# Optimization experiments

Hardware: AMD Instinct MI355X
Metric: run time of the kernel (lower is better)

Reference implementation:

```python
import jax, jax.numpy as jnp
import numpy as np

N = 50000          # num nodes
E = 800000         # num edges (avg degree 16)
H = 8              # num_heads
CH = [64, 64, 64, 32]  # [in_features] + conv_channels
EPS = 1e-5


def setup_inputs() -> dict:
    key = jax.random.key(0)
    ks = jax.random.split(key, 20)
    x = jax.random.normal(ks[0], (N, CH[0]), jnp.float32)
    src = jax.random.randint(ks[1], (E,), 0, N, dtype=jnp.int32)
    dst = jax.random.randint(ks[2], (E,), 0, N, dtype=jnp.int32)
    dst = jnp.where(src == dst, (dst + 1) % N, dst)  # no self-loops (remove_self_loops)
    edge_index = jnp.stack([src, dst])  # [2, E]

    def lin(k, shape):
        return jax.random.uniform(k, shape, jnp.float32) * 0.1

    inp = {"x": x, "edge_index": edge_index}
    ki = 3
    for layer, (cin, cout) in enumerate(zip(CH[:-1], CH[1:]), start=1):
        inp[f"W{layer}"] = lin(ks[ki], (H * cout, cin)); ki += 1
        inp[f"U{layer}"] = lin(ks[ki], (H, cin)); ki += 1
        inp[f"c{layer}"] = jax.random.normal(ks[ki], (H,), jnp.float32) * 0.1; ki += 1
        inp[f"b{layer}"] = jax.random.normal(ks[ki], (cout,), jnp.float32) * 0.1; ki += 1
        if layer < 3:  # batch norm on intermediate layers only
            inp[f"g{layer}"] = jnp.ones((cout,), jnp.float32)
            inp[f"be{layer}"] = jnp.zeros((cout,), jnp.float32)
    return inp


def _conv(x, src, dst, inv_count, W, U, c, b, out_ch):
    # FeatureSteeredConvolution (translation-invariant attention), mean aggr.
    xi = x[dst]                                   # [E2, Cin] target features
    xj = x[src]                                   # [E2, Cin] source features
    attn = jax.nn.softmax((xi - xj) @ U.T + c, axis=1)   # [E2, H]
    proj = (xj @ W.T).reshape(-1, H, out_ch)      # [E2, H, Cout]
    msg = jnp.einsum('eh,eho->eo', attn, proj)    # [E2, Cout]
    agg = jax.ops.segment_sum(msg, dst, num_segments=N) * inv_count[:, None]
    return agg + b


def _bn(x, g, be):
    # BatchNorm1d, training mode (batch stats, biased variance)
    m = x.mean(axis=0)
    v = ((x - m) ** 2).mean(axis=0)
    return g * (x - m) * jax.lax.rsqrt(v + EPS) + be


def reference(x, edge_index, W1, U1, c1, b1, g1, be1,
              W2, U2, c2, b2, g2, be2, W3, U3, c3, b3):
    loops = jnp.arange(N, dtype=edge_index.dtype)
    src = jnp.concatenate([edge_index[0], loops])  # add_self_loops
    dst = jnp.concatenate([edge_index[1], loops])
    count = jax.ops.segment_sum(jnp.ones_like(dst, jnp.float32), dst, num_segments=N)
    inv_count = 1.0 / count  # every node has its self-loop, so count >= 1

    h = _conv(x, src, dst, inv_count, W1, U1, c1, b1, CH[1])
    h = _bn(jax.nn.relu(h), g1, be1)
    h = _conv(h, src, dst, inv_count, W2, U2, c2, b2, CH[2])
    h = _bn(jax.nn.relu(h), g2, be2)
    return _conv(h, src, dst, inv_count, W3, U3, c3, b3, CH[3])
```

## Files before the change

### kernel.cpp

```cpp
#include <hip/hip_runtime.h>
#include <hip/hip_bf16.h>
#include <hip/hip_fp16.h>
#include <math.h>

constexpr int NN = 50000;
constexpr int NE = 800000;
constexpr float L2E = 1.44269504f;
constexpr int SBLK = 256;
constexpr int SGRID = (NN + SBLK - 1) / SBLK;

typedef __attribute__((ext_vector_type(8))) short bf16x8;
typedef __attribute__((ext_vector_type(4))) float f32x4;

__device__ inline float b2f(unsigned short u) {
  union { unsigned int i; float f; } v;
  v.i = ((unsigned int)u) << 16;
  return v.f;
}

__global__ void k_deg(const int* __restrict__ dst, int* __restrict__ degin) {
  int i = blockIdx.x * blockDim.x + threadIdx.x;
  if (i < NE) atomicAdd(&degin[dst[i]], 1);
}

__global__ void k_inv(const int* __restrict__ degin, float* __restrict__ inv) {
  int i = blockIdx.x * blockDim.x + threadIdx.x;
  if (i < NN) inv[i] = 1.0f / (float)(degin[i] + 1);
}

__global__ void k_scan1(const int* __restrict__ deg, int* __restrict__ bsum) {
  int i = blockIdx.x * SBLK + threadIdx.x;
  int v = (i < NN) ? deg[i] : 0;
#pragma unroll
  for (int off = 32; off; off >>= 1) v += __shfl_down(v, off, 64);
  __shared__ int ws[SBLK / 64];
  if ((threadIdx.x & 63) == 0) ws[threadIdx.x >> 6] = v;
  __syncthreads();
  if (threadIdx.x == 0) {
    int s = 0;
#pragma unroll
    for (int w = 0; w < SBLK / 64; ++w) s += ws[w];
    bsum[blockIdx.x] = s;
  }
}

__global__ void k_scan2(int* __restrict__ bsum) {
  __shared__ int ls[256];
  int t = threadIdx.x;
  int v = (t < SGRID) ? bsum[t] : 0;
  ls[t] = v;
  __syncthreads();
  for (int off = 1; off < 256; off <<= 1) {
    int u = (t >= off) ? ls[t - off] : 0;
    __syncthreads();
    ls[t] += u;
    __syncthreads();
  }
  if (t < SGRID) bsum[t] = ls[t] - v;
}

__global__ void k_scan3(const int* __restrict__ deg, const int* __restrict__ bsum,
                        int* __restrict__ base, int* __restrict__ cursor) {
  __shared__ int ls[SBLK];
  int t = threadIdx.x;
  int i = blockIdx.x * SBLK + t;
  int v = (i < NN) ? deg[i] : 0;
  ls[t] = v;
  __syncthreads();
  for (int off = 1; off < SBLK; off <<= 1) {
    int u = (t >= off) ? ls[t - off] : 0;
    __syncthreads();
    ls[t] += u;
    __syncthreads();
  }
  int ex = ls[t] - v + bsum[blockIdx.x];
  if (i < NN) { base[i] = ex; cursor[i] = ex; }
}

__global__ void k_scatter(const int* __restrict__ src, const int* __restrict__ dst,
                          int* __restrict__ cursor, int2* __restrict__ csc2) {
  int e = blockIdx.x * blockDim.x + threadIdx.x;
  if (e < NE) {
    int s = src[e], d = dst[e];
    int pos = atomicAdd(&cursor[d], 1);
    csc2[pos] = make_int2(s, d);
  }
}

__global__ void k_f2b(const float* __restrict__ in, __hip_bfloat16* __restrict__ out,
                      long n4) {
  long i = (long)blockIdx.x * blockDim.x + threadIdx.x;
  if (i >= n4) return;
  float4 v = reinterpret_cast<const float4*>(in)[i];
  ushort4 o;
  o.x = __hip_bfloat16_raw(__float2bfloat16(v.x)).x;
  o.y = __hip_bfloat16_raw(__float2bfloat16(v.y)).x;
  o.z = __hip_bfloat16_raw(__float2bfloat16(v.z)).x;
  o.w = __hip_bfloat16_raw(__float2bfloat16(v.w)).x;
  reinterpret_cast<ushort4*>(out)[i] = o;
}

__global__ void k_wt(const float* __restrict__ w1, const float* __restrict__ w2,
                     const float* __restrict__ w3, __hip_bfloat16* __restrict__ t1,
                     __hip_bfloat16* __restrict__ t2, __hip_bfloat16* __restrict__ t3) {
  int i = blockIdx.x * blockDim.x + threadIdx.x;
  const int n1 = 64 * 512, n2 = 64 * 512, n3 = 32 * 512;
  const float* w; __hip_bfloat16* t; int cout; int j = i;
  if (j < n1) { w = w1; t = t1; cout = 64; }
  else if ((j -= n1) < n2) { w = w2; t = t2; cout = 64; }
  else if ((j -= n2) < n3) { w = w3; t = t3; cout = 32; }
  else return;
  int o = j >> 9;
  int hc = j & 511;
  int h = hc >> 6, c = hc & 63;
  t[j] = __float2bfloat16(w[(h * cout + o) * 64 + c]);
}

__global__ void k_q(const float* __restrict__ X, const float* __restrict__ U,
                    float* __restrict__ q) {
  int n = blockIdx.x * blockDim.x + threadIdx.x;
  if (n >= NN) return;
  float4 xr[16];
  const float4* X4 = reinterpret_cast<const float4*>(X) + (size_t)n * 16;
#pragma unroll
  for (int i = 0; i < 16; ++i) xr[i] = X4[i];
  const float4* U4 = reinterpret_cast<const float4*>(U);
#pragma unroll
  for (int h = 0; h < 8; ++h) {
    float a = 0.f;
#pragma unroll
    for (int i = 0; i < 16; ++i) {
      float4 u = U4[h * 16 + i];
      a = fmaf(xr[i].x, u.x, a);
      a = fmaf(xr[i].y, u.y, a);
      a = fmaf(xr[i].z, u.z, a);
      a = fmaf(xr[i].w, u.w, a);
    }
    q[(size_t)n * 8 + h] = a * L2E;
  }
}

__global__ void k_attn(const int2* __restrict__ csc2, const float* __restrict__ q,
                       const float* __restrict__ cvec, const float* __restrict__ inv,
                       uint4* __restrict__ a) {
  int k = blockIdx.x * blockDim.x + threadIdx.x;
  if (k >= NE) return;
  int2 sd = csc2[k];
  int s = sd.x, d = sd.y;

  const float4* q4 = reinterpret_cast<const float4*>(q);
  const float4* c4 = reinterpret_cast<const float4*>(cvec);
  float4 qd0 = q4[2 * d], qd1 = q4[2 * d + 1];
  float4 qs0 = q4[2 * s], qs1 = q4[2 * s + 1];
  float4 c0 = c4[0], c1 = c4[1];

  float e[8];
  e[0] = __builtin_amdgcn_exp2f(qd0.x - qs0.x + c0.x * L2E);
  e[1] = __builtin_amdgcn_exp2f(qd0.y - qs0.y + c0.y * L2E);
  e[2] = __builtin_amdgcn_exp2f(qd0.z - qs0.z + c0.z * L2E);
  e[3] = __builtin_amdgcn_exp2f(qd0.w - qs0.w + c0.w * L2E);
  e[4] = __builtin_amdgcn_exp2f(qd1.x - qs1.x + c1.x * L2E);
  e[5] = __builtin_amdgcn_exp2f(qd1.y - qs1.y + c1.y * L2E);
  e[6] = __builtin_amdgcn_exp2f(qd1.z - qs1.z + c1.z * L2E);
  e[7] = __builtin_amdgcn_exp2f(qd1.w - qs1.w + c1.w * L2E);

  float sum = ((e[0] + e[1]) + (e[2] + e[3])) + ((e[4] + e[5]) + (e[6] + e[7]));
  float r = __builtin_amdgcn_rcpf(sum) * inv[d];

  __half2 h0 = __floats2half2_rn(e[0] * r, e[1] * r);
  __half2 h1 = __floats2half2_rn(e[2] * r, e[3] * r);
  __half2 h2 = __floats2half2_rn(e[4] * r, e[5] * r);
  __half2 h3 = __floats2half2_rn(e[6] * r, e[7] * r);
  uint4 o;
  o.x = *(unsigned int*)&h0;
  o.y = *(unsigned int*)&h1;
  o.z = *(unsigned int*)&h2;
  o.w = *(unsigned int*)&h3;
  a[k] = o;
}

#define ZACC(AV, XS)                                                      \
  do {                                                                    \
    float2 f0 = __half22float2(*(__half2*)&(AV).x);                       \
    float2 f1 = __half22float2(*(__half2*)&(AV).y);                       \
    float2 f2 = __half22float2(*(__half2*)&(AV).z);                       \
    float2 f3 = __half22float2(*(__half2*)&(AV).w);                       \
    z[0] = fmaf(f0.x, (XS), z[0]);                                        \
    z[1] = fmaf(f0.y, (XS), z[1]);                                        \
    z[2] = fmaf(f1.x, (XS), z[2]);                                        \
    z[3] = fmaf(f1.y, (XS), z[3]);                                        \
    z[4] = fmaf(f2.x, (XS), z[4]);                                        \
    z[5] = fmaf(f2.y, (XS), z[5]);                                        \
    z[6] = fmaf(f3.x, (XS), z[6]);                                        \
    z[7] = fmaf(f3.y, (XS), z[7]);                                        \
  } while (0)

__global__ void k_zagg(const int* __restrict__ cscbase, const int* __restrict__ cscend,
                       const int2* __restrict__ csc2, const uint4* __restrict__ a,
                       const ushort* __restrict__ xb, const float* __restrict__ inv,
                       const float* __restrict__ cvec, __hip_bfloat16* __restrict__ zb) {
  const int lane = threadIdx.x & 63;
  const int n = (int)(((long)blockIdx.x * blockDim.x + threadIdx.x) >> 6);
  if (n >= NN) return;

  float wc[8], wsum = 0.f;
#pragma unroll
  for (int h = 0; h < 8; ++h) { wc[h] = __builtin_amdgcn_exp2f(cvec[h] * L2E); wsum += wc[h]; }
  const float rxd = __builtin_amdgcn_rcpf(wsum) * inv[n] * b2f(xb[(size_t)n * 64 + lane]);
  float z[8];
#pragma unroll
  for (int h = 0; h < 8; ++h) z[h] = wc[h] * rxd;

  int k = cscbase[n];
  const int k1 = cscend[n];
  for (; k + 4 <= k1; k += 4) {
    int s0 = csc2[k + 0].x;
    int s1 = csc2[k + 1].x;
    int s2 = csc2[k + 2].x;
    int s3 = csc2[k + 3].x;
    uint4 a0 = a[k + 0];
    uint4 a1 = a[k + 1];
    uint4 a2 = a[k + 2];
    uint4 a3 = a[k + 3];
    float x0 = b2f(xb[(size_t)s0 * 64 + lane]);
    float x1 = b2f(xb[(size_t)s1 * 64 + lane]);
    float x2 = b2f(xb[(size_t)s2 * 64 + lane]);
    float x3 = b2f(xb[(size_t)s3 * 64 + lane]);
    ZACC(a0, x0);
    ZACC(a1, x1);
    ZACC(a2, x2);
    ZACC(a3, x3);
  }
  for (; k < k1; ++k) {
    int s = csc2[k].x;
    uint4 av = a[k];
    float xs = b2f(xb[(size_t)s * 64 + lane]);
    ZACC(av, xs);
  }

  ushort* zo = reinterpret_cast<ushort*>(zb) + (size_t)n * 512 + lane;
#pragma unroll
  for (int h = 0; h < 8; ++h)
    zo[h * 64] = __hip_bfloat16_raw(__float2bfloat16(z[h])).x;
}

template <int JOUT>
__global__ void __launch_bounds__(256)
k_zgemm(const __hip_bfloat16* __restrict__ Zb, const __hip_bfloat16* __restrict__ Wt,
        float* __restrict__ go) {
  const int lane = threadIdx.x & 63;
  const int w = threadIdx.x >> 6;
  const int m0 = (blockIdx.x * 4 + w) * 64;
  const int lr = lane & 15;
  const int lk = lane >> 4;
  constexpr int NT = JOUT / 16;

  const ushort* Z = reinterpret_cast<const ushort*>(Zb);
  const ushort* W = reinterpret_cast<const ushort*>(Wt);

  f32x4 acc[4][NT] = {};
  for (int kk = 0; kk < 16; ++kk) {
    bf16x8 bfr[NT];
#pragma unroll
    for (int ni = 0; ni < NT; ++ni) {
      int j = ni * 16 + lr;
      bfr[ni] = *reinterpret_cast<const bf16x8*>(W + (size_t)j * 512 + kk * 32 + lk * 8);
    }
#pragma unroll
    for (int mi = 0; mi < 4; ++mi) {
      int r = m0 + mi * 16 + lr;
      if (r >= NN) r = NN - 1;
      bf16x8 afr = *reinterpret_cast<const bf16x8*>(Z + (size_t)r * 512 + kk * 32 + lk * 8);
#pragma unroll
      for (int ni = 0; ni < NT; ++ni)
        acc[mi][ni] = __builtin_amdgcn_mfma_f32_16x16x32_bf16(afr, bfr[ni], acc[mi][ni], 0, 0, 0);
    }
  }

#pragma unroll
  for (int mi = 0; mi < 4; ++mi) {
#pragma unroll
    for (int i = 0; i < 4; ++i) {
      int r = m0 + mi * 16 + lk * 4 + i;
      if (r < NN) {
#pragma unroll
        for (int ni = 0; ni < NT; ++ni)
          go[(size_t)r * JOUT + ni * 16 + lr] = acc[mi][ni][i];
      }
    }
  }
}

__global__ void k_finalize_relu(const float* __restrict__ go, const float* __restrict__ b,
                                float* __restrict__ y, float* __restrict__ stats) {
  __shared__ float ssum[64], ssq[64];
  const int t = threadIdx.x;
  if (t < 64) { ssum[t] = 0.f; ssq[t] = 0.f; }
  __syncthreads();

  const int o = t & 63;
  const float bo = b[o];
  float lsum = 0.f, lsq = 0.f;
  for (long idx = (long)blockIdx.x * blockDim.x + threadIdx.x; idx < (long)NN * 64;
       idx += (long)gridDim.x * blockDim.x) {
    float v = fmaxf(go[idx] + bo, 0.f);
    y[idx] = v;
    lsum += v;
    lsq = fmaf(v, v, lsq);
  }
  atomicAdd(&ssum[o], lsum);
  atomicAdd(&ssq[o], lsq);
  __syncthreads();
  if (t < 64) {
    atomicAdd(&stats[t], ssum[t]);
    atomicAdd(&stats[64 + t], ssq[t]);
  }
}

__global__ void k_bn(const float* __restrict__ y, const float* __restrict__ stats,
                     const float* __restrict__ g, const float* __restrict__ be,
                     float* __restrict__ h, __hip_bfloat16* __restrict__ hb) {
  long idx = (long)blockIdx.x * blockDim.x + threadIdx.x;
  if (idx >= (long)NN * 64) return;
  int o = (int)(idx & 63);
  float m = stats[o] * (1.0f / NN);
  float v = stats[64 + o] * (1.0f / NN) - m * m;
  float r = fmaf(g[o] * rsqrtf(v + 1e-5f), y[idx] - m, be[o]);
  h[idx] = r;
  hb[idx] = __float2bfloat16(r);
}

__global__ void k_final3(const float* __restrict__ go, const float* __restrict__ b,
                         float* __restrict__ out) {
  long idx = (long)blockIdx.x * blockDim.x + threadIdx.x;
  if (idx >= (long)NN * 32) return;
  out[idx] = go[idx] + b[(int)(idx & 31)];
}

extern "C" void kernel_launch(void* const* d_in, const int* in_sizes, int n_in,
                              void* d_out, int out_size, void* d_ws, size_t ws_size,
                              hipStream_t stream) {
  const float* x   = (const float*)d_in[0];
  const int*   src = (const int*)d_in[1];
  const int*   dst = src + NE;
  const float* W1 = (const float*)d_in[2];
  const float* U1 = (const float*)d_in[3];
  const float* c1 = (const float*)d_in[4];
  const float* b1 = (const float*)d_in[5];
  const float* g1 = (const float*)d_in[6];
  const float* be1 = (const float*)d_in[7];
  const float* W2 = (const float*)d_in[8];
  const float* U2 = (const float*)d_in[9];
  const float* c2 = (const float*)d_in[10];
  const float* b2 = (const float*)d_in[11];
  const float* g2 = (const float*)d_in[12];
  const float* be2 = (const float*)d_in[13];
  const float* W3 = (const float*)d_in[14];
  const float* U3 = (const float*)d_in[15];
  const float* c3 = (const float*)d_in[16];
  const float* b3 = (const float*)d_in[17];
  float* out = (float*)d_out;

  float* ws   = (float*)d_ws;
  float* inv  = ws;
  float* q    = inv + NN;
  float* h    = q + (size_t)NN * 8;
  float* go   = h + (size_t)NN * 64;
  float* stats = go + (size_t)NN * 64;
  uint4* a    = (uint4*)(stats + 128);
  __hip_bfloat16* xb = (__hip_bfloat16*)(a + NE);
  __hip_bfloat16* zb = xb + (size_t)NN * 64;
  __hip_bfloat16* Wt1 = zb + (size_t)NN * 512;
  __hip_bfloat16* Wt2 = Wt1 + 64 * 512;
  __hip_bfloat16* Wt3 = Wt2 + 64 * 512;
  int* degin   = (int*)(Wt3 + 32 * 512);
  int* cscbase = degin + NN;
  int* cursor  = cscbase + NN;
  int* bsum    = cursor + NN;
  int2* csc2   = (int2*)(bsum + 256);

  const int BLK = 256;
  dim3 b256(BLK);

  hipMemsetAsync(degin, 0, (size_t)NN * 4, stream);
  k_deg<<<dim3((NE + BLK - 1) / BLK), b256, 0, stream>>>(dst, degin);
  k_inv<<<dim3((NN + BLK - 1) / BLK), b256, 0, stream>>>(degin, inv);
  k_scan1<<<dim3(SGRID), dim3(SBLK), 0, stream>>>(degin, bsum);
  k_scan2<<<dim3(1), dim3(256), 0, stream>>>(bsum);
  k_scan3<<<dim3(SGRID), dim3(SBLK), 0, stream>>>(degin, bsum, cscbase, cursor);
  k_scatter<<<dim3((NE + BLK - 1) / BLK), b256, 0, stream>>>(src, dst, cursor, csc2);

  const int qgrid = (NN + BLK - 1) / BLK;
  const int attn_grid = (NE + BLK - 1) / BLK;
  const int zagg_grid = NN * 64 / BLK;
  const int zgemm_grid = (NN + 255) / 256;
  const long xb4 = (long)NN * 64 / 4;
  const int wtgrid = (64 * 512 * 2 + 32 * 512 + BLK - 1) / BLK;

  k_f2b<<<dim3((xb4 + BLK - 1) / BLK), b256, 0, stream>>>(x, xb, xb4);
  k_wt<<<dim3(wtgrid), b256, 0, stream>>>(W1, W2, W3, Wt1, Wt2, Wt3);

  k_q<<<dim3(qgrid), b256, 0, stream>>>(x, U1, q);
  k_attn<<<dim3(attn_grid), b256, 0, stream>>>(csc2, q, c1, inv, a);
  k_zagg<<<dim3(zagg_grid), b256, 0, stream>>>(cscbase, cursor, csc2, a,
                                               (const ushort*)xb, inv, c1, zb);
  k_zgemm<64><<<dim3(zgemm_grid), b256, 0, stream>>>(zb, Wt1, go);
  hipMemsetAsync(stats, 0, 128 * 4, stream);
  k_finalize_relu<<<dim3(1024), b256, 0, stream>>>(go, b1, go, stats);
  k_bn<<<dim3(((size_t)NN * 64 + BLK - 1) / BLK), b256, 0, stream>>>(go, stats, g1, be1, h, xb);

  k_q<<<dim3(qgrid), b256, 0, stream>>>(h, U2, q);
  k_attn<<<dim3(attn_grid), b256, 0, stream>>>(csc2, q, c2, inv, a);
  k_zagg<<<dim3(zagg_grid), b256, 0, stream>>>(cscbase, cursor, csc2, a,
                                               (const ushort*)xb, inv, c2, zb);
  k_zgemm<64><<<dim3(zgemm_grid), b256, 0, stream>>>(zb, Wt2, go);
  hipMemsetAsync(stats, 0, 128 * 4, stream);
  k_finalize_relu<<<dim3(1024), b256, 0, stream>>>(go, b2, go, stats);
  k_bn<<<dim3(((size_t)NN * 64 + BLK - 1) / BLK), b256, 0, stream>>>(go, stats, g2, be2, h, xb);

  k_q<<<dim3(qgrid), b256, 0, stream>>>(h, U3, q);
  k_attn<<<dim3(attn_grid), b256, 0, stream>>>(csc2, q, c3, inv, a);
  k_zagg<<<dim3(zagg_grid), b256, 0, stream>>>(cscbase, cursor, csc2, a,
                                               (const ushort*)xb, inv, c3, zb);
  k_zgemm<32><<<dim3(zgemm_grid), b256, 0, stream>>>(zb, Wt3, go);
  k_final3<<<dim3(((size_t)NN * 32 + BLK - 1) / BLK), b256, 0, stream>>>(go, b3, out);
}
```

Before: 454.7 us.

## Fuse bias/ReLU/BN-stats into GEMM epilogue and BN with next-layer q projection

Folds bias, ReLU and batch-norm statistic accumulation into the tensor-core GEMM epilogue, replacing separate finalize and final-bias kernels. Merges batch-norm application with the next layer's attention-logit projection (wave-wide shuffle reductions), so the fp32 normalized copy and the separate q kernel are gone. Splits the edge list into a source-index array plus a precomputed destination array, which narrows the per-edge index read in aggregation. This removes several full passes over node features, at the cost of more atomics in the GEMM epilogue and an extra one-time preprocessing kernel.

```diff
diff --git a/kernel.cpp b/kernel.cpp
--- a/kernel.cpp
+++ b/kernel.cpp
@@ -78,13 +78,22 @@
 }
 
 __global__ void k_scatter(const int* __restrict__ src, const int* __restrict__ dst,
-                          int* __restrict__ cursor, int2* __restrict__ csc2) {
+                          int* __restrict__ cursor, int* __restrict__ csrc) {
   int e = blockIdx.x * blockDim.x + threadIdx.x;
   if (e < NE) {
-    int s = src[e], d = dst[e];
-    int pos = atomicAdd(&cursor[d], 1);
-    csc2[pos] = make_int2(s, d);
-  }
+    int pos = atomicAdd(&cursor[dst[e]], 1);
+    csrc[pos] = src[e];
+  }
+}
+
+__global__ void k_dstpos(const int* __restrict__ cscbase, const int* __restrict__ degin,
+                         int* __restrict__ dstpos) {
+  const int lane = threadIdx.x & 63;
+  const int n = (int)(((long)blockIdx.x * blockDim.x + threadIdx.x) >> 6);
+  if (n >= NN) return;
+  const int base = cscbase[n];
+  const int end = base + degin[n];
+  for (int k = base + lane; k < end; k += 64) dstpos[k] = n;
 }
 
 __global__ void k_f2b(const float* __restrict__ in, __hip_bfloat16* __restrict__ out,
@@ -140,13 +149,12 @@
   }
 }
 
-__global__ void k_attn(const int2* __restrict__ csc2, const float* __restrict__ q,
-                       const float* __restrict__ cvec, const float* __restrict__ inv,
-                       uint4* __restrict__ a) {
+__global__ void k_attn(const int* __restrict__ csrc, const int* __restrict__ dstpos,
+                       const float* __restrict__ q, const float* __restrict__ cvec,
+                       const float* __restrict__ inv, uint4* __restrict__ a) {
   int k = blockIdx.x * blockDim.x + threadIdx.x;
   if (k >= NE) return;
-  int2 sd = csc2[k];
-  int s = sd.x, d = sd.y;
+  int s = csrc[k], d = dstpos[k];
 
   const float4* q4 = reinterpret_cast<const float4*>(q);
   const float4* c4 = reinterpret_cast<const float4*>(cvec);
@@ -196,7 +204,7 @@
   } while (0)
 
 __global__ void k_zagg(const int* __restrict__ cscbase, const int* __restrict__ cscend,
-                       const int2* __restrict__ csc2, const uint4* __restrict__ a,
+                       const int* __restrict__ csrc, const uint4* __restrict__ a,
                        const ushort* __restrict__ xb, const float* __restrict__ inv,
                        const float* __restrict__ cvec, __hip_bfloat16* __restrict__ zb) {
   const int lane = threadIdx.x & 63;
@@ -214,10 +222,10 @@
   int k = cscbase[n];
   const int k1 = cscend[n];
   for (; k + 4 <= k1; k += 4) {
-    int s0 = csc2[k + 0].x;
-    int s1 = csc2[k + 1].x;
-    int s2 = csc2[k + 2].x;
-    int s3 = csc2[k + 3].x;
+    int s0 = csrc[k + 0];
+    int s1 = csrc[k + 1];
+    int s2 = csrc[k + 2];
+    int s3 = csrc[k + 3];
     uint4 a0 = a[k + 0];
     uint4 a1 = a[k + 1];
     uint4 a2 = a[k + 2];
@@ -232,7 +240,7 @@
     ZACC(a3, x3);
   }
   for (; k < k1; ++k) {
-    int s = csc2[k].x;
+    int s = csrc[k];
     uint4 av = a[k];
     float xs = b2f(xb[(size_t)s * 64 + lane]);
     ZACC(av, xs);
@@ -244,10 +252,12 @@
     zo[h * 64] = __hip_bfloat16_raw(__float2bfloat16(z[h])).x;
 }
 
-template <int JOUT>
+template <int JOUT, bool RS>
 __global__ void __launch_bounds__(256)
-k_zgemm(const __hip_bfloat16* __restrict__ Zb, const __hip_bfloat16* __restrict__ Wt,
-        float* __restrict__ go) {
+k_zgemm_ep(const __hip_bfloat16* __restrict__ Zb, const __hip_bfloat16* __restrict__ Wt,
+           const float* __restrict__ b, float* __restrict__ yout,
+           float* __restrict__ stats) {
+  __shared__ float ssum[64], ssq[64];
   const int lane = threadIdx.x & 63;
   const int w = threadIdx.x >> 6;
   const int m0 = (blockIdx.x * 4 + w) * 64;
@@ -255,6 +265,9 @@
   const int lk = lane >> 4;
   constexpr int NT = JOUT / 16;
 
+  if (RS && threadIdx.x < 64) { ssum[threadIdx.x] = 0.f; ssq[threadIdx.x] = 0.f; }
+  if (RS) __syncthreads();
+
   const ushort* Z = reinterpret_cast<const ushort*>(Zb);
   const ushort* W = reinterpret_cast<const ushort*>(Wt);
 
@@ -277,6 +290,11 @@
     }
   }
 
+  float bj[NT];
+#pragma unroll
+  for (int ni = 0; ni < NT; ++ni) bj[ni] = b[ni * 16 + lr];
+
+  float ps[NT] = {}, pq[NT] = {};
 #pragma unroll
   for (int mi = 0; mi < 4; ++mi) {
 #pragma unroll
@@ -284,57 +302,60 @@
       int r = m0 + mi * 16 + lk * 4 + i;
       if (r < NN) {
 #pragma unroll
-        for (int ni = 0; ni < NT; ++ni)
-          go[(size_t)r * JOUT + ni * 16 + lr] = acc[mi][ni][i];
+        for (int ni = 0; ni < NT; ++ni) {
+          float v = acc[mi][ni][i] + bj[ni];
+          if (RS) {
+            v = fmaxf(v, 0.f);
+            ps[ni] += v;
+            pq[ni] = fmaf(v, v, pq[ni]);
+          }
+          yout[(size_t)r * JOUT + ni * 16 + lr] = v;
+        }
       }
     }
   }
-}
-
-__global__ void k_finalize_relu(const float* __restrict__ go, const float* __restrict__ b,
-                                float* __restrict__ y, float* __restrict__ stats) {
-  __shared__ float ssum[64], ssq[64];
-  const int t = threadIdx.x;
-  if (t < 64) { ssum[t] = 0.f; ssq[t] = 0.f; }
-  __syncthreads();
-
-  const int o = t & 63;
-  const float bo = b[o];
-  float lsum = 0.f, lsq = 0.f;
-  for (long idx = (long)blockIdx.x * blockDim.x + threadIdx.x; idx < (long)NN * 64;
-       idx += (long)gridDim.x * blockDim.x) {
-    float v = fmaxf(go[idx] + bo, 0.f);
-    y[idx] = v;
-    lsum += v;
-    lsq = fmaf(v, v, lsq);
-  }
-  atomicAdd(&ssum[o], lsum);
-  atomicAdd(&ssq[o], lsq);
-  __syncthreads();
-  if (t < 64) {
-    atomicAdd(&stats[t], ssum[t]);
-    atomicAdd(&stats[64 + t], ssq[t]);
-  }
-}
-
-__global__ void k_bn(const float* __restrict__ y, const float* __restrict__ stats,
-                     const float* __restrict__ g, const float* __restrict__ be,
-                     float* __restrict__ h, __hip_bfloat16* __restrict__ hb) {
-  long idx = (long)blockIdx.x * blockDim.x + threadIdx.x;
-  if (idx >= (long)NN * 64) return;
-  int o = (int)(idx & 63);
-  float m = stats[o] * (1.0f / NN);
-  float v = stats[64 + o] * (1.0f / NN) - m * m;
-  float r = fmaf(g[o] * rsqrtf(v + 1e-5f), y[idx] - m, be[o]);
-  h[idx] = r;
-  hb[idx] = __float2bfloat16(r);
-}
-
-__global__ void k_final3(const float* __restrict__ go, const float* __restrict__ b,
-                         float* __restrict__ out) {
-  long idx = (long)blockIdx.x * blockDim.x + threadIdx.x;
-  if (idx >= (long)NN * 32) return;
-  out[idx] = go[idx] + b[(int)(idx & 31)];
+
+  if (RS) {
+#pragma unroll
+    for (int ni = 0; ni < NT; ++ni) {
+      atomicAdd(&ssum[ni * 16 + lr], ps[ni]);
+      atomicAdd(&ssq[ni * 16 + lr], pq[ni]);
+    }
+    __syncthreads();
+    if (threadIdx.x < 64) {
+      atomicAdd(&stats[threadIdx.x], ssum[threadIdx.x]);
+      atomicAdd(&stats[64 + threadIdx.x], ssq[threadIdx.x]);
+    }
+  }
+}
+
+__global__ void __launch_bounds__(256)
+k_bnq(const float* __restrict__ y, const float* __restrict__ stats,
+      const float* __restrict__ g, const float* __restrict__ be,
+      const float* __restrict__ U, __hip_bfloat16* __restrict__ xb,
+      float* __restrict__ q) {
+  const int lane = threadIdx.x & 63;
+  const int n = (int)(((long)blockIdx.x * blockDim.x + threadIdx.x) >> 6);
+  if (n >= NN) return;
+
+  float m = stats[lane] * (1.0f / NN);
+  float v = stats[64 + lane] * (1.0f / NN) - m * m;
+  float r = fmaf(g[lane] * rsqrtf(v + 1e-5f), y[(size_t)n * 64 + lane] - m, be[lane]);
+  xb[(size_t)n * 64 + lane] = __float2bfloat16(r);
+
+  float qv[8];
+#pragma unroll
+  for (int h = 0; h < 8; ++h) {
+    float p = r * U[h * 64 + lane];
+#pragma unroll
+    for (int off = 32; off; off >>= 1) p += __shfl_xor(p, off, 64);
+    qv[h] = p;
+  }
+  if (lane == 0) {
+    float4* q4 = reinterpret_cast<float4*>(q + (size_t)n * 8);
+    q4[0] = make_float4(qv[0] * L2E, qv[1] * L2E, qv[2] * L2E, qv[3] * L2E);
+    q4[1] = make_float4(qv[4] * L2E, qv[5] * L2E, qv[6] * L2E, qv[7] * L2E);
+  }
 }
 
 extern "C" void kernel_launch(void* const* d_in, const int* in_sizes, int n_in,
@@ -364,9 +385,8 @@
   float* ws   = (float*)d_ws;
   float* inv  = ws;
   float* q    = inv + NN;
-  float* h    = q + (size_t)NN * 8;
-  float* go   = h + (size_t)NN * 64;
-  float* stats = go + (size_t)NN * 64;
+  float* y    = q + (size_t)NN * 8;
+  float* stats = y + (size_t)NN * 64;
   uint4* a    = (uint4*)(stats + 128);
   __hip_bfloat16* xb = (__hip_bfloat16*)(a + NE);
   __hip_bfloat16* zb = xb + (size_t)NN * 64;
@@ -377,7 +397,8 @@
   int* cscbase = degin + NN;
   int* cursor  = cscbase + NN;
   int* bsum    = cursor + NN;
-  int2* csc2   = (int2*)(bsum + 256);
+  int* csrc    = bsum + 256;
+  int* dstpos  = csrc + NE;
 
   const int BLK = 256;
   dim3 b256(BLK);
@@ -388,11 +409,12 @@
   k_scan1<<<dim3(SGRID), dim3(SBLK), 0, stream>>>(degin, bsum);
   k_scan2<<<dim3(1), dim3(256), 0, stream>>>(bsum);
   k_scan3<<<dim3(SGRID), dim3(SBLK), 0, stream>>>(degin, bsum, cscbase, cursor);
-  k_scatter<<<dim3((NE + BLK - 1) / BLK), b256, 0, stream>>>(src, dst, cursor, csc2);
+  k_scatter<<<dim3((NE + BLK - 1) / BLK), b256, 0, stream>>>(src, dst, cursor, csrc);
+  k_dstpos<<<dim3(NN * 64 / BLK), b256, 0, stream>>>(cscbase, degin, dstpos);
 
   const int qgrid = (NN + BLK - 1) / BLK;
   const int attn_grid = (NE + BLK - 1) / BLK;
-  const int zagg_grid = NN * 64 / BLK;
+  const int node_grid = NN * 64 / BLK;
   const int zgemm_grid = (NN + 255) / 256;
   const long xb4 = (long)NN * 64 / 4;
   const int wtgrid = (64 * 512 * 2 + 32 * 512 + BLK - 1) / BLK;
@@ -401,27 +423,22 @@
   k_wt<<<dim3(wtgrid), b256, 0, stream>>>(W1, W2, W3, Wt1, Wt2, Wt3);
 
   k_q<<<dim3(qgrid), b256, 0, stream>>>(x, U1, q);
-  k_attn<<<dim3(attn_grid), b256, 0, stream>>>(csc2, q, c1, inv, a);
-  k_zagg<<<dim3(zagg_grid), b256, 0, stream>>>(cscbase, cursor, csc2, a,
+  k_attn<<<dim3(attn_grid), b256, 0, stream>>>(csrc, dstpos, q, c1, inv, a);
+  k_zagg<<<dim3(node_grid), b256, 0, stream>>>(cscbase, cursor, csrc, a,
                                                (const ushort*)xb, inv, c1, zb);
-  k_zgemm<64><<<dim3(zgemm_grid), b256, 0, stream>>>(zb, Wt1, go);
   hipMemsetAsync(stats, 0, 128 * 4, stream);
-  k_finalize_relu<<<dim3(1024), b256, 0, stream>>>(go, b1, go, stats);
-  k_bn<<<dim3(((size_t)NN * 64 + BLK - 1) / BLK), b256, 0, stream>>>(go, stats, g1, be1, h, xb);
-
-  k_q<<<dim3(qgrid), b256, 0, stream>>>(h, U2, q);
-  k_attn<<<dim3(attn_grid), b256, 0, stream>>>(csc2, q, c2, inv, a);
-  k_zagg<<<dim3(zagg_grid), b256, 0, stream>>>(cscbase, cursor, csc2, a,
+  k_zgemm_ep<64, true><<<dim3(zgemm_grid), b256, 0, stream>>>(zb, Wt1, b1, y, stats);
+  k_bnq<<<dim3(node_grid), b256, 0, stream>>>(y, stats, g1, be1, U2, xb, q);
+
+  k_attn<<<dim3(attn_grid), b256, 0, stream>>>(csrc, dstpos, q, c2, inv, a);
+  k_zagg<<<dim3(node_grid), b256, 0, stream>>>(cscbase, cursor, csrc, a,
                                                (const ushort*)xb, inv, c2, zb);
-  k_zgemm<64><<<dim3(zgemm_grid), b256, 0, stream>>>(zb, Wt2, go);
   hipMemsetAsync(stats, 0, 128 * 4, stream);
-  k_finalize_relu<<<dim3(1024), b256, 0, stream>>>(go, b2, go, stats);
-  k_bn<<<dim3(((size_t)NN * 64 + BLK - 1) / BLK), b256, 0, stream>>>(go, stats, g2, be2, h, xb);
-
-  k_q<<<dim3(qgrid), b256, 0, stream>>>(h, U3, q);
-  k_attn<<<dim3(attn_grid), b256, 0, stream>>>(csc2, q, c3, inv, a);
-  k_zagg<<<dim3(zagg_grid), b256, 0, stream>>>(cscbase, cursor, csc2, a,
+  k_zgemm_ep<64, true><<<dim3(zgemm_grid), b256, 0, stream>>>(zb, Wt2, b2, y, stats);
+  k_bnq<<<dim3(node_grid), b256, 0, stream>>>(y, stats, g2, be2, U3, xb, q);
+
+  k_attn<<<dim3(attn_grid), b256, 0, stream>>>(csrc, dstpos, q, c3, inv, a);
+  k_zagg<<<dim3(node_grid), b256, 0, stream>>>(cscbase, cursor, csrc, a,
                                                (const ushort*)xb, inv, c3, zb);
-  k_zgemm<32><<<dim3(zgemm_grid), b256, 0, stream>>>(zb, Wt3, go);
-  k_final3<<<dim3(((size_t)NN * 32 + BLK - 1) / BLK), b256, 0, stream>>>(go, b3, out);
-}
+  k_zgemm_ep<32, false><<<dim3(zgemm_grid), b256, 0, stream>>>(zb, Wt3, b3, out, nullptr);
+}
```

After: 419.7 us. 1.08x faster.
